# Performance work log

Measured on AMD Instinct MI355X. Metric: run time of the kernel, lower is better.

The kernel has to match this reference:

```python
import jax, jax.numpy as jnp
import numpy as np

D_MODEL = 1024
NUM_EXPERTS = 16
TOP_K = 2
TOP_C = 4  # min(E, max(4, 2*top_k))
TAU = 1.0
RANK = 64  # max(4, d_model // 16)


def _stable_softmax(v):
    m = jnp.max(v, axis=-1, keepdims=True)
    e = jnp.exp(v - m)
    return e / (jnp.sum(e, axis=-1, keepdims=True) + 1e-12)


def setup_inputs() -> dict:
    key = jax.random.key(0)
    ks = jax.random.split(key, 8)
    B, D, E, R = 16384, D_MODEL, NUM_EXPERTS, RANK
    x = jax.random.normal(ks[0], (B, D), dtype=jnp.float32)
    W_enc = jax.random.normal(ks[1], (D, D), dtype=jnp.float32) * (1.0 / np.sqrt(D))
    b_enc = jnp.zeros((D,), dtype=jnp.float32)
    W_gate = jax.random.normal(ks[2], (E, D), dtype=jnp.float32) * (1.0 / np.sqrt(D))
    U = jax.random.normal(ks[3], (E, R, D), dtype=jnp.float32) * (1.0 / np.sqrt(D))
    V = jax.random.normal(ks[4], (E, D, R), dtype=jnp.float32) * (1.0 / np.sqrt(R))
    gamma = jnp.ones((E,), dtype=jnp.float32)
    return {"x": x, "W_enc": W_enc, "b_enc": b_enc, "W_gate": W_gate,
            "U": U, "V": V, "gamma": gamma}


def reference(x, W_enc, b_enc, W_gate, U, V, gamma):
    # shared encoder
    encoded = x @ W_enc.T + b_enc                      # [B, D]
    # gating: logits -> top_c -> top_k -> softmax over selected logits
    logits = (encoded @ W_gate.T) / TAU                # [B, E]
    topc_vals, topc_idx = jax.lax.top_k(logits, TOP_C)
    topk_vals, pos_in_c = jax.lax.top_k(topc_vals, TOP_K)
    topk_idx = jnp.take_along_axis(topc_idx, pos_in_c, axis=1)  # [B, K]
    topk_w = _stable_softmax(topk_vals)                # [B, K], all > 1e-12
    # dense per-(token, expert) combine weight (equivalent to gather/scatter)
    B = x.shape[0]
    w_dense = jnp.zeros((B, NUM_EXPERTS), dtype=x.dtype)
    w_dense = w_dense.at[jnp.arange(B)[:, None], topk_idx].add(topk_w)
    # low-rank experts: delta_e(x) = gamma_e * silu(x U_e^T) V_e^T
    s = jax.nn.silu(jnp.einsum('bd,erd->ber', encoded, U))        # [B, E, R]
    coef = w_dense * gamma[None, :]                               # [B, E]
    delta = jnp.einsum('ber,edr->bd', s * coef[..., None], V)     # [B, D]
    # y = encoded + sum_k w_k * (expert(x) - x)  with expert(x)-x = delta_e
    return encoded + delta
```

## Files before the change

### kernel.cpp

```cpp
#include <hip/hip_runtime.h>
#include <hip/hip_bf16.h>

#define D_DIM 1024
#define NE 16
#define RK 64
#define NTOK 16384

typedef __bf16 bf16;
typedef __bf16 bf16x8 __attribute__((ext_vector_type(8)));
typedef __bf16 bf16x4 __attribute__((ext_vector_type(4)));
typedef float f32x4 __attribute__((ext_vector_type(4)));

__device__ __forceinline__ void gload16(const void* g, void* l) {
  __builtin_amdgcn_global_load_lds((const __attribute__((address_space(1))) unsigned int*)g,
                                   (__attribute__((address_space(3))) unsigned int*)l,
                                   16, 0, 0);
}

__global__ void k_cast(const float* __restrict__ s, bf16* __restrict__ d, int n4) {
  int i = blockIdx.x * blockDim.x + threadIdx.x;
  if (i >= n4) return;
  float4 v = ((const float4*)s)[i];
  bf16x4 o = { (bf16)v.x, (bf16)v.y, (bf16)v.z, (bf16)v.w };
  ((bf16x4*)d)[i] = o;
}

__global__ void k_castv(const float* __restrict__ V, bf16* __restrict__ Vb2) {
  int id = blockIdx.x * 256 + threadIdx.x;
  int d = id & 1023;
  int rb = (id >> 10) & 7;
  int e = id >> 13;
  const float* src = V + ((size_t)(e * 1024 + d)) * 64 + rb * 8;
  float4 v0 = *(const float4*)src;
  float4 v1 = *(const float4*)(src + 4);
  bf16x8 o = { (bf16)v0.x, (bf16)v0.y, (bf16)v0.z, (bf16)v0.w,
               (bf16)v1.x, (bf16)v1.y, (bf16)v1.z, (bf16)v1.w };
  *(bf16x8*)(Vb2 + (size_t)id * 8) = o;
}

__global__ void k_gmat(const float* __restrict__ Wg, const float* __restrict__ We,
                       float* __restrict__ Gt2) {
  int d = blockIdx.x * 256 + threadIdx.x;
  int e = blockIdx.y;
  int j0 = blockIdx.z * 128;
  double a0 = 0.0, a1 = 0.0, a2 = 0.0, a3 = 0.0;
  for (int j = j0; j < j0 + 128; j += 4) {
    a0 += (double)Wg[e * D_DIM + j + 0] * (double)We[(size_t)(j + 0) * D_DIM + d];
    a1 += (double)Wg[e * D_DIM + j + 1] * (double)We[(size_t)(j + 1) * D_DIM + d];
    a2 += (double)Wg[e * D_DIM + j + 2] * (double)We[(size_t)(j + 2) * D_DIM + d];
    a3 += (double)Wg[e * D_DIM + j + 3] * (double)We[(size_t)(j + 3) * D_DIM + d];
  }
  atomicAdd(&Gt2[(d >> 2) * 64 + e * 4 + (d & 3)], (float)((a0 + a1) + (a2 + a3)));
}

__global__ void k_bgate(const float* __restrict__ Wg, const float* __restrict__ be,
                        float* __restrict__ bg) {
  __shared__ double red[256];
  int e = blockIdx.x, t = threadIdx.x;
  double a = 0.0;
  for (int j = t; j < D_DIM; j += 256) a += (double)Wg[e * D_DIM + j] * (double)be[j];
  red[t] = a; __syncthreads();
  for (int s = 128; s > 0; s >>= 1) { if (t < s) red[t] += red[t + s]; __syncthreads(); }
  if (t == 0) bg[e] = (float)red[0];
}

__global__ __launch_bounds__(256) void k_gatecast(const float* __restrict__ x,
                                                  const float* __restrict__ Gt2,
                                                  const float* __restrict__ bg,
                                                  const float* __restrict__ gamma,
                                                  bf16* __restrict__ xb,
                                                  int* __restrict__ pk,
                                                  float2* __restrict__ wpair) {
  __shared__ float bufx[8][1024];
  __shared__ float Ls[4 * 2 * NE];
  int tid = threadIdx.x;
  int wv = tid >> 6, lane = tid & 63;
  int g = lane & 15;
  int s = lane >> 4;
  int tokbase = blockIdx.x * 8 + wv * 2;

  const float* xr0 = x + (size_t)tokbase * D_DIM;
#pragma unroll
  for (int c = 0; c < 4; ++c) {
    gload16(xr0 + c * 256 + lane * 4, &bufx[wv * 2][c * 256 + lane * 4]);
    gload16(xr0 + D_DIM + c * 256 + lane * 4, &bufx[wv * 2 + 1][c * 256 + lane * 4]);
  }

  const float* Gq = Gt2 + s * 64 + g * 4;
  const float* b0p = &bufx[wv * 2][s * 4];
  const float* b1p = &bufx[wv * 2 + 1][s * 4];
  float acc0 = 0.0f, acc1 = 0.0f;
  float4 gv = *(const float4*)Gq;
  for (int it = 0; it < 64; ++it) {
    int nx = (it < 63) ? it + 1 : 0;
    float4 gn = *(const float4*)(Gq + (size_t)nx * 256);
    float4 x0 = *(const float4*)(b0p + it * 16);
    float4 x1 = *(const float4*)(b1p + it * 16);
    acc0 += x0.x * gv.x + x0.y * gv.y + x0.z * gv.z + x0.w * gv.w;
    acc1 += x1.x * gv.x + x1.y * gv.y + x1.z * gv.z + x1.w * gv.w;
    gv = gn;
  }
  acc0 += __shfl_xor(acc0, 16); acc0 += __shfl_xor(acc0, 32);
  acc1 += __shfl_xor(acc1, 16); acc1 += __shfl_xor(acc1, 32);
  if (s == 0) {
    Ls[wv * 32 + g] = acc0;
    Ls[wv * 32 + 16 + g] = acc1;
  }

#pragma unroll
  for (int t = 0; t < 2; ++t) {
    const float4* src = (const float4*)&bufx[wv * 2 + t][0];
    bf16x4* dst = (bf16x4*)(xb + (size_t)(tokbase + t) * D_DIM);
#pragma unroll
    for (int r = 0; r < 4; ++r) {
      float4 v = src[lane + 64 * r];
      bf16x4 o = { (bf16)v.x, (bf16)v.y, (bf16)v.z, (bf16)v.w };
      dst[lane + 64 * r] = o;
    }
  }
  __syncthreads();

  if (lane < 2) {
    int t = lane;
    int tok = tokbase + t;
    const float* lrow = &Ls[wv * 32 + t * 16];
    float v1 = -1e30f, v2 = -1e30f; int i1 = 0, i2 = 0;
#pragma unroll
    for (int e = 0; e < NE; ++e) {
      float v = lrow[e] + bg[e];
      if (v > v1) { v2 = v1; i2 = i1; v1 = v; i1 = e; }
      else if (v > v2) { v2 = v; i2 = e; }
    }
    float e1 = expf(v2 - v1);
    float den = 1.0f + e1 + 1e-12f;
    float w0 = (1.0f / den) * gamma[i1];
    float w1 = (e1 / den) * gamma[i2];
    pk[tok] = i1 | (i2 << 8);
    wpair[tok] = make_float2(w0, w1);
  }
}

__global__ __launch_bounds__(256) void k_scatter(const int* __restrict__ pk,
                                                 const float2* __restrict__ wpair,
                                                 int* __restrict__ cnt,
                                                 int* __restrict__ lists,
                                                 float* __restrict__ wl) {
  __shared__ int lc[32];
  __shared__ int base[32];
  __shared__ int lc2[32];
  int tid = threadIdx.x;
  int tok = blockIdx.x * 256 + tid;
  if (tid < 32) { lc[tid] = 0; lc2[tid] = 0; }
  __syncthreads();
  int p = pk[tok];
  float2 w = wpair[tok];
  int b0 = p & 0xff;
  int b1 = 16 + ((p >> 8) & 0xff);
  atomicAdd(&lc[b0], 1);
  atomicAdd(&lc[b1], 1);
  __syncthreads();
  if (tid < 32 && lc[tid] > 0) base[tid] = atomicAdd(&cnt[tid], lc[tid]);
  __syncthreads();
  int r0 = base[b0] + atomicAdd(&lc2[b0], 1);
  lists[(size_t)b0 * NTOK + r0] = tok;
  wl[(size_t)b0 * NTOK + r0] = w.x;
  int r1 = base[b1] + atomicAdd(&lc2[b1], 1);
  lists[(size_t)b1 * NTOK + r1] = tok;
  wl[(size_t)b1 * NTOK + r1] = w.y;
}

__global__ void k_btab(const int* __restrict__ cnt, int2* __restrict__ btab,
                       int* __restrict__ nblk) {
  int lane = threadIdx.x;
  int nb = (lane < 32) ? ((cnt[lane] + 63) >> 6) : 0;
  int pfx = nb;
  for (int off = 1; off < 32; off <<= 1) {
    int v = __shfl_up(pfx, off);
    if (lane >= off) pfx += v;
  }
  int start = pfx - nb;
  if (lane < 32) {
    int c = cnt[lane];
    int i = 0;
    for (int t0 = 0; t0 < c; t0 += 64, ++i)
      btab[start + i] = make_int2(lane, t0);
  }
  if (lane == 31) *nblk = pfx;
}

__global__ __launch_bounds__(512, 1) void k_encgemm(const bf16* __restrict__ A,
                                                    const bf16* __restrict__ W,
                                                    const float* __restrict__ bias,
                                                    bf16* __restrict__ encb) {
  __shared__ bf16 As[256 * 64];
  __shared__ bf16 Bs[256 * 64];
  int tid = threadIdx.x;
  int w = blockIdx.x;
  int bm = (w & 63) * 256;
  int bn = (w >> 6) * 256;
  int lane = tid & 63, wv = tid >> 6;
  int wm = (wv >> 2) * 128, wn = (wv & 3) * 64;
  int srow = tid >> 3;
  int sc = tid & 7;
  int cs = sc ^ (srow & 7);
  int fr = lane & 15, fk = (lane >> 4) * 8;
  f32x4 acc[8][4] = {};
  for (int k0 = 0; k0 < D_DIM; k0 += 64) {
    __syncthreads();
#pragma unroll
    for (int p = 0; p < 4; ++p) {
      int r = p * 64 + srow;
      gload16(A + (size_t)(bm + r) * D_DIM + k0 + cs * 8, &As[r * 64 + sc * 8]);
    }
#pragma unroll
    for (int p = 0; p < 4; ++p) {
      int r = p * 64 + srow;
      gload16(W + (size_t)(bn + r) * D_DIM + k0 + cs * 8, &Bs[r * 64 + sc * 8]);
    }
    __syncthreads();
#pragma unroll
    for (int kk = 0; kk < 2; ++kk) {
      bf16x8 af[8], bv[4];
#pragma unroll
      for (int m = 0; m < 8; ++m) {
        int row = wm + m * 16 + fr;
        af[m] = *(const bf16x8*)&As[(row * 64 + kk * 32 + fk) ^ ((row & 7) << 3)];
      }
#pragma unroll
      for (int n = 0; n < 4; ++n) {
        int row = wn + n * 16 + fr;
        bv[n] = *(const bf16x8*)&Bs[(row * 64 + kk * 32 + fk) ^ ((row & 7) << 3)];
      }
#pragma unroll
      for (int m = 0; m < 8; ++m)
#pragma unroll
        for (int n = 0; n < 4; ++n)
          acc[m][n] = __builtin_amdgcn_mfma_f32_16x16x32_bf16(af[m], bv[n], acc[m][n], 0, 0, 0);
    }
  }
  int rg = (lane >> 4) * 4;
#pragma unroll
  for (int n = 0; n < 4; ++n) {
    int col = bn + wn + n * 16 + fr;
    float bval = bias[col];
#pragma unroll
    for (int m = 0; m < 8; ++m) {
#pragma unroll
      for (int r = 0; r < 4; ++r) {
        int row = bm + wm + m * 16 + rg + r;
        encb[(size_t)row * D_DIM + col] = (bf16)(acc[m][n][r] + bval);
      }
    }
  }
}

__global__ __launch_bounds__(256) void k_expert(const bf16* __restrict__ encb,
                                                const bf16* __restrict__ Ub,
                                                const bf16* __restrict__ Vb2,
                                                const int* __restrict__ cnt,
                                                const int* __restrict__ lists,
                                                const float* __restrict__ wl,
                                                const int2* __restrict__ btab,
                                                const int* __restrict__ nblk,
                                                bf16* __restrict__ d0,
                                                bf16* __restrict__ d1) {
  int bid = blockIdx.x;
  if (bid >= *nblk) return;
  int2 bt = btab[bid];
  int bin = bt.x, t0 = bt.y;
  int slot = bin >> 4, e = bin & 15;
  int c = cnt[bin];
  int nrows = c - t0; if (nrows > 64) nrows = 64;
  const int* tl = lists + (size_t)bin * NTOK + t0;
  const float* wlp = wl + (size_t)bin * NTOK + t0;

  __shared__ int toks[64];
  __shared__ float coefs[64];
  __shared__ bf16 As[64 * 64];
  __shared__ bf16 Us[64 * 64];
  __shared__ bf16 Ss[64 * 64];

  int tid = threadIdx.x;
  if (tid < 64) {
    int rr = tid < nrows ? tid : nrows - 1;
    toks[tid] = tl[rr];
    coefs[tid] = tid < nrows ? wlp[tid] : 0.0f;
  }
  __syncthreads();

  int lane = tid & 63, wv = tid >> 6;
  int srow = tid >> 3, scol = (tid & 7) * 8;
  int fr = lane & 15, fk = (lane >> 4) * 8;
  size_t tokA0 = (size_t)toks[srow] * D_DIM;
  size_t tokA1 = (size_t)toks[32 + srow] * D_DIM;
  const bf16* Ue = Ub + (size_t)e * RK * D_DIM;
  f32x4 acc1[4] = {};

  for (int k0 = 0; k0 < D_DIM; k0 += 64) {
    __syncthreads();
    gload16(encb + tokA0 + k0 + scol, &As[srow * 64 + scol]);
    gload16(encb + tokA1 + k0 + scol, &As[(32 + srow) * 64 + scol]);
    gload16(Ue + (size_t)srow * D_DIM + k0 + scol, &Us[srow * 64 + scol]);
    gload16(Ue + (size_t)(32 + srow) * D_DIM + k0 + scol, &Us[(32 + srow) * 64 + scol]);
    __syncthreads();
#pragma unroll
    for (int kk = 0; kk < 2; ++kk) {
      bf16x8 af = *(const bf16x8*)&As[(wv * 16 + fr) * 64 + kk * 32 + fk];
#pragma unroll
      for (int n = 0; n < 4; ++n) {
        bf16x8 bv = *(const bf16x8*)&Us[(n * 16 + fr) * 64 + kk * 32 + fk];
        acc1[n] = __builtin_amdgcn_mfma_f32_16x16x32_bf16(af, bv, acc1[n], 0, 0, 0);
      }
    }
  }
  int rg = (lane >> 4) * 4;
#pragma unroll
  for (int n = 0; n < 4; ++n)
#pragma unroll
    for (int r = 0; r < 4; ++r) {
      int row = wv * 16 + rg + r;
      float v = acc1[n][r];
      float s = v / (1.0f + __expf(-v));
      Ss[row * 64 + n * 16 + fr] = (bf16)(s * coefs[row]);
    }
  __syncthreads();
  bf16x8 a2[4][2];
#pragma unroll
  for (int m = 0; m < 4; ++m)
#pragma unroll
    for (int kk = 0; kk < 2; ++kk)
      a2[m][kk] = *(const bf16x8*)&Ss[(m * 16 + fr) * 64 + kk * 32 + fk];

  const bf16* Ve2 = Vb2 + (size_t)e * RK * D_DIM;
  bf16* dst = slot ? d1 : d0;
  int rb0 = lane >> 4;
  int colbase = wv * 256;
  for (int nj = 0; nj < 16; ++nj) {
    int dcol = colbase + nj * 16 + fr;
    bf16x8 b0 = *(const bf16x8*)&Ve2[((size_t)rb0 * D_DIM + dcol) * 8];
    bf16x8 b1 = *(const bf16x8*)&Ve2[((size_t)(rb0 + 4) * D_DIM + dcol) * 8];
#pragma unroll
    for (int m = 0; m < 4; ++m) {
      f32x4 a = {};
      a = __builtin_amdgcn_mfma_f32_16x16x32_bf16(a2[m][0], b0, a, 0, 0, 0);
      a = __builtin_amdgcn_mfma_f32_16x16x32_bf16(a2[m][1], b1, a, 0, 0, 0);
#pragma unroll
      for (int r = 0; r < 4; ++r) {
        int row = m * 16 + rg + r;
        if (row < nrows) {
          dst[(size_t)toks[row] * D_DIM + dcol] = (bf16)a[r];
        }
      }
    }
  }
}

__global__ __launch_bounds__(256) void k_final(float* __restrict__ out,
                                               const bf16* __restrict__ encb,
                                               const bf16* __restrict__ d0,
                                               const bf16* __restrict__ d1) {
  size_t i = ((size_t)blockIdx.x * 256 + threadIdx.x) * 8;
  bf16x8 e = *(const bf16x8*)(encb + i);
  bf16x8 a = *(const bf16x8*)(d0 + i);
  bf16x8 b = *(const bf16x8*)(d1 + i);
  float4 o0, o1;
  o0.x = (float)e[0] + (float)a[0] + (float)b[0];
  o0.y = (float)e[1] + (float)a[1] + (float)b[1];
  o0.z = (float)e[2] + (float)a[2] + (float)b[2];
  o0.w = (float)e[3] + (float)a[3] + (float)b[3];
  o1.x = (float)e[4] + (float)a[4] + (float)b[4];
  o1.y = (float)e[5] + (float)a[5] + (float)b[5];
  o1.z = (float)e[6] + (float)a[6] + (float)b[6];
  o1.w = (float)e[7] + (float)a[7] + (float)b[7];
  *(float4*)(out + i) = o0;
  *(float4*)(out + i + 4) = o1;
}

extern "C" void kernel_launch(void* const* d_in, const int* in_sizes, int n_in,
                              void* d_out, int out_size, void* d_ws, size_t ws_size,
                              hipStream_t stream) {
  const float* x   = (const float*)d_in[0];
  const float* We  = (const float*)d_in[1];
  const float* be  = (const float*)d_in[2];
  const float* Wg  = (const float*)d_in[3];
  const float* U   = (const float*)d_in[4];
  const float* V   = (const float*)d_in[5];
  const float* gam = (const float*)d_in[6];
  float* out = (float*)d_out;
  char* ws = (char*)d_ws;

  int*    cnt  = (int*)(ws + 0);
  float*  Gt2  = (float*)(ws + 256);
  float*  bg   = (float*)(ws + 66048);
  int2*   btab = (int2*)(ws + 66176);
  int*    nblk = (int*)(ws + 70656);
  bf16*   xb   = (bf16*)(ws + 131072);
  bf16*   d0   = (bf16*)(ws + 131072);
  bf16*   encb = (bf16*)(ws + 131072 + 33554432);
  char*   base = ws + 131072 + 2 * 33554432;
  bf16*   Wb   = (bf16*)(base);
  bf16*   Ubf  = (bf16*)(base + 2097152);
  bf16*   Vb2  = (bf16*)(base + 2 * 2097152);
  int*    lists= (int*)(base + 3 * 2097152);
  float*  wl   = (float*)(base + 4 * 2097152);
  int*    pk   = (int*)(base + 5 * 2097152);
  float2* wpr  = (float2*)(base + 5 * 2097152 + 131072);
  bf16*   d1   = (bf16*)(base + 5 * 2097152 + 131072 + 131072 + 131072);

  hipMemsetAsync(ws, 0, 66048, stream);

  k_cast<<<1024, 256, 0, stream>>>(We, Wb, 1048576 / 4);
  k_cast<<<1024, 256, 0, stream>>>(U, Ubf, 1048576 / 4);
  k_castv<<<512, 256, 0, stream>>>(V, Vb2);

  dim3 gg(4, 16, 8);
  k_gmat<<<gg, 256, 0, stream>>>(Wg, We, Gt2);
  k_bgate<<<16, 256, 0, stream>>>(Wg, be, bg);

  k_gatecast<<<2048, 256, 0, stream>>>(x, Gt2, bg, gam, xb, pk, wpr);
  k_scatter<<<64, 256, 0, stream>>>(pk, wpr, cnt, lists, wl);
  k_btab<<<1, 64, 0, stream>>>(cnt, btab, nblk);

  k_encgemm<<<256, 512, 0, stream>>>(xb, Wb, be, encb);

  k_expert<<<544, 256, 0, stream>>>(encb, Ubf, Vb2, cnt, lists, wl, btab, nblk, d0, d1);
  k_final<<<8192, 256, 0, stream>>>(out, encb, d0, d1);
}
```

Before: 183.8 us.

## Double-buffer encoder and expert GEMMs, stage epilogue stores through LDS

The encoder GEMM now uses a 32-wide K step with two LDS buffers, so global-to-LDS loads for the next tile are issued before the MFMAs on the current tile, and the XOR swizzle is dropped. The expert kernel gets a double-buffered, swizzled first GEMM. Both epilogues stage bf16 results in padded per-wave LDS tiles so global writes become vectorized row-contiguous stores instead of scattered 2-byte stores. The aim is to hide load latency and cut store transactions, at the cost of more LDS per block and possible bank conflicts from the unswizzled 32-wide encoder tiles.

```diff
diff --git a/kernel.cpp b/kernel.cpp
--- a/kernel.cpp
+++ b/kernel.cpp
@@ -192,64 +192,78 @@
                                                     const bf16* __restrict__ W,
                                                     const float* __restrict__ bias,
                                                     bf16* __restrict__ encb) {
-  __shared__ bf16 As[256 * 64];
-  __shared__ bf16 Bs[256 * 64];
+  __shared__ char smem[65536];
+  bf16* const AsB = (bf16*)smem;
+  bf16* const BsB = (bf16*)(smem + 32768);
   int tid = threadIdx.x;
   int w = blockIdx.x;
   int bm = (w & 63) * 256;
   int bn = (w >> 6) * 256;
   int lane = tid & 63, wv = tid >> 6;
   int wm = (wv >> 2) * 128, wn = (wv & 3) * 64;
-  int srow = tid >> 3;
-  int sc = tid & 7;
-  int cs = sc ^ (srow & 7);
+  int srow = tid >> 2;
+  int sc = (tid & 3) * 8;
   int fr = lane & 15, fk = (lane >> 4) * 8;
   f32x4 acc[8][4] = {};
-  for (int k0 = 0; k0 < D_DIM; k0 += 64) {
+
+  {
+    bf16* as = AsB; bf16* bs = BsB;
+    gload16(A + (size_t)(bm + srow) * D_DIM + sc, &as[srow * 32 + sc]);
+    gload16(A + (size_t)(bm + 128 + srow) * D_DIM + sc, &as[(128 + srow) * 32 + sc]);
+    gload16(W + (size_t)(bn + srow) * D_DIM + sc, &bs[srow * 32 + sc]);
+    gload16(W + (size_t)(bn + 128 + srow) * D_DIM + sc, &bs[(128 + srow) * 32 + sc]);
+  }
+  __syncthreads();
+
+  for (int k0 = 0; k0 < D_DIM; k0 += 32) {
+    int cur = (k0 >> 5) & 1;
+    if (k0 + 32 < D_DIM) {
+      int kn = k0 + 32;
+      bf16* as = AsB + (cur ^ 1) * 8192;
+      bf16* bs = BsB + (cur ^ 1) * 8192;
+      gload16(A + (size_t)(bm + srow) * D_DIM + kn + sc, &as[srow * 32 + sc]);
+      gload16(A + (size_t)(bm + 128 + srow) * D_DIM + kn + sc, &as[(128 + srow) * 32 + sc]);
+      gload16(W + (size_t)(bn + srow) * D_DIM + kn + sc, &bs[srow * 32 + sc]);
+      gload16(W + (size_t)(bn + 128 + srow) * D_DIM + kn + sc, &bs[(128 + srow) * 32 + sc]);
+    }
+    const bf16* as = AsB + cur * 8192;
+    const bf16* bs = BsB + cur * 8192;
+    bf16x8 af[8], bv[4];
+#pragma unroll
+    for (int m = 0; m < 8; ++m)
+      af[m] = *(const bf16x8*)&as[(wm + m * 16 + fr) * 32 + fk];
+#pragma unroll
+    for (int n = 0; n < 4; ++n)
+      bv[n] = *(const bf16x8*)&bs[(wn + n * 16 + fr) * 32 + fk];
+#pragma unroll
+    for (int m = 0; m < 8; ++m)
+#pragma unroll
+      for (int n = 0; n < 4; ++n)
+        acc[m][n] = __builtin_amdgcn_mfma_f32_16x16x32_bf16(af[m], bv[n], acc[m][n], 0, 0, 0);
     __syncthreads();
-#pragma unroll
-    for (int p = 0; p < 4; ++p) {
-      int r = p * 64 + srow;
-      gload16(A + (size_t)(bm + r) * D_DIM + k0 + cs * 8, &As[r * 64 + sc * 8]);
-    }
-#pragma unroll
-    for (int p = 0; p < 4; ++p) {
-      int r = p * 64 + srow;
-      gload16(W + (size_t)(bn + r) * D_DIM + k0 + cs * 8, &Bs[r * 64 + sc * 8]);
-    }
-    __syncthreads();
-#pragma unroll
-    for (int kk = 0; kk < 2; ++kk) {
-      bf16x8 af[8], bv[4];
-#pragma unroll
-      for (int m = 0; m < 8; ++m) {
-        int row = wm + m * 16 + fr;
-        af[m] = *(const bf16x8*)&As[(row * 64 + kk * 32 + fk) ^ ((row & 7) << 3)];
+  }
+
+  int rg = (lane >> 4) * 4;
+  bf16* tb = (bf16*)smem + wv * 2176;
+#pragma unroll
+  for (int h = 0; h < 4; ++h) {
+#pragma unroll
+    for (int mi = 0; mi < 2; ++mi) {
+      int m = h * 2 + mi;
+#pragma unroll
+      for (int n = 0; n < 4; ++n) {
+        float bval = bias[bn + wn + n * 16 + fr];
+#pragma unroll
+        for (int r = 0; r < 4; ++r)
+          tb[(mi * 16 + rg + r) * 68 + n * 16 + fr] = (bf16)(acc[m][n][r] + bval);
       }
-#pragma unroll
-      for (int n = 0; n < 4; ++n) {
-        int row = wn + n * 16 + fr;
-        bv[n] = *(const bf16x8*)&Bs[(row * 64 + kk * 32 + fk) ^ ((row & 7) << 3)];
-      }
-#pragma unroll
-      for (int m = 0; m < 8; ++m)
-#pragma unroll
-        for (int n = 0; n < 4; ++n)
-          acc[m][n] = __builtin_amdgcn_mfma_f32_16x16x32_bf16(af[m], bv[n], acc[m][n], 0, 0, 0);
-    }
-  }
-  int rg = (lane >> 4) * 4;
-#pragma unroll
-  for (int n = 0; n < 4; ++n) {
-    int col = bn + wn + n * 16 + fr;
-    float bval = bias[col];
-#pragma unroll
-    for (int m = 0; m < 8; ++m) {
-#pragma unroll
-      for (int r = 0; r < 4; ++r) {
-        int row = bm + wm + m * 16 + rg + r;
-        encb[(size_t)row * D_DIM + col] = (bf16)(acc[m][n][r] + bval);
-      }
+    }
+#pragma unroll
+    for (int it2 = 0; it2 < 8; ++it2) {
+      int row = it2 * 4 + (lane >> 4);
+      int c4 = (lane & 15) * 4;
+      *(ushort4*)&encb[(size_t)(bm + wm + h * 32 + row) * D_DIM + bn + wn + c4] =
+        *(const ushort4*)&tb[row * 68 + c4];
     }
   }
 }
@@ -276,9 +290,10 @@
 
   __shared__ int toks[64];
   __shared__ float coefs[64];
-  __shared__ bf16 As[64 * 64];
-  __shared__ bf16 Us[64 * 64];
+  __shared__ bf16 As[2][64 * 64];
+  __shared__ bf16 Us[2][64 * 64];
   __shared__ bf16 Ss[64 * 64];
+  __shared__ bf16 xtrb[4][64 * 34];
 
   int tid = threadIdx.x;
   if (tid < 64) {
@@ -289,30 +304,45 @@
   __syncthreads();
 
   int lane = tid & 63, wv = tid >> 6;
-  int srow = tid >> 3, scol = (tid & 7) * 8;
+  int srow = tid >> 3;
+  int sc8 = tid & 7;
+  int cs = (sc8 ^ (srow & 7)) * 8;
+  int scol = sc8 * 8;
   int fr = lane & 15, fk = (lane >> 4) * 8;
   size_t tokA0 = (size_t)toks[srow] * D_DIM;
   size_t tokA1 = (size_t)toks[32 + srow] * D_DIM;
   const bf16* Ue = Ub + (size_t)e * RK * D_DIM;
   f32x4 acc1[4] = {};
 
+  gload16(encb + tokA0 + cs, &As[0][srow * 64 + scol]);
+  gload16(encb + tokA1 + cs, &As[0][(32 + srow) * 64 + scol]);
+  gload16(Ue + (size_t)srow * D_DIM + cs, &Us[0][srow * 64 + scol]);
+  gload16(Ue + (size_t)(32 + srow) * D_DIM + cs, &Us[0][(32 + srow) * 64 + scol]);
+  __syncthreads();
+
   for (int k0 = 0; k0 < D_DIM; k0 += 64) {
-    __syncthreads();
-    gload16(encb + tokA0 + k0 + scol, &As[srow * 64 + scol]);
-    gload16(encb + tokA1 + k0 + scol, &As[(32 + srow) * 64 + scol]);
-    gload16(Ue + (size_t)srow * D_DIM + k0 + scol, &Us[srow * 64 + scol]);
-    gload16(Ue + (size_t)(32 + srow) * D_DIM + k0 + scol, &Us[(32 + srow) * 64 + scol]);
-    __syncthreads();
+    int cur = (k0 >> 6) & 1;
+    if (k0 + 64 < D_DIM) {
+      int kn = k0 + 64;
+      gload16(encb + tokA0 + kn + cs, &As[cur ^ 1][srow * 64 + scol]);
+      gload16(encb + tokA1 + kn + cs, &As[cur ^ 1][(32 + srow) * 64 + scol]);
+      gload16(Ue + (size_t)srow * D_DIM + kn + cs, &Us[cur ^ 1][srow * 64 + scol]);
+      gload16(Ue + (size_t)(32 + srow) * D_DIM + kn + cs, &Us[cur ^ 1][(32 + srow) * 64 + scol]);
+    }
+    int arow = wv * 16 + fr;
+    int sw = (fr & 7) << 3;
 #pragma unroll
     for (int kk = 0; kk < 2; ++kk) {
-      bf16x8 af = *(const bf16x8*)&As[(wv * 16 + fr) * 64 + kk * 32 + fk];
+      bf16x8 af = *(const bf16x8*)&As[cur][(arow * 64 + kk * 32 + fk) ^ sw];
 #pragma unroll
       for (int n = 0; n < 4; ++n) {
-        bf16x8 bv = *(const bf16x8*)&Us[(n * 16 + fr) * 64 + kk * 32 + fk];
+        bf16x8 bv = *(const bf16x8*)&Us[cur][((n * 16 + fr) * 64 + kk * 32 + fk) ^ sw];
         acc1[n] = __builtin_amdgcn_mfma_f32_16x16x32_bf16(af, bv, acc1[n], 0, 0, 0);
       }
     }
-  }
+    __syncthreads();
+  }
+
   int rg = (lane >> 4) * 4;
 #pragma unroll
   for (int n = 0; n < 4; ++n)
@@ -335,22 +365,31 @@
   bf16* dst = slot ? d1 : d0;
   int rb0 = lane >> 4;
   int colbase = wv * 256;
-  for (int nj = 0; nj < 16; ++nj) {
-    int dcol = colbase + nj * 16 + fr;
-    bf16x8 b0 = *(const bf16x8*)&Ve2[((size_t)rb0 * D_DIM + dcol) * 8];
-    bf16x8 b1 = *(const bf16x8*)&Ve2[((size_t)(rb0 + 4) * D_DIM + dcol) * 8];
-#pragma unroll
-    for (int m = 0; m < 4; ++m) {
-      f32x4 a = {};
-      a = __builtin_amdgcn_mfma_f32_16x16x32_bf16(a2[m][0], b0, a, 0, 0, 0);
-      a = __builtin_amdgcn_mfma_f32_16x16x32_bf16(a2[m][1], b1, a, 0, 0, 0);
-#pragma unroll
-      for (int r = 0; r < 4; ++r) {
-        int row = m * 16 + rg + r;
-        if (row < nrows) {
-          dst[(size_t)toks[row] * D_DIM + dcol] = (bf16)a[r];
-        }
+  bf16* tb = xtrb[wv];
+  for (int njb = 0; njb < 8; ++njb) {
+#pragma unroll
+    for (int nj2 = 0; nj2 < 2; ++nj2) {
+      int nj = njb * 2 + nj2;
+      int dcol = colbase + nj * 16 + fr;
+      bf16x8 b0 = *(const bf16x8*)&Ve2[((size_t)rb0 * D_DIM + dcol) * 8];
+      bf16x8 b1 = *(const bf16x8*)&Ve2[((size_t)(rb0 + 4) * D_DIM + dcol) * 8];
+#pragma unroll
+      for (int m = 0; m < 4; ++m) {
+        f32x4 a = {};
+        a = __builtin_amdgcn_mfma_f32_16x16x32_bf16(a2[m][0], b0, a, 0, 0, 0);
+        a = __builtin_amdgcn_mfma_f32_16x16x32_bf16(a2[m][1], b1, a, 0, 0, 0);
+#pragma unroll
+        for (int r = 0; r < 4; ++r)
+          tb[(m * 16 + rg + r) * 34 + nj2 * 16 + fr] = (bf16)a[r];
       }
+    }
+#pragma unroll
+    for (int it2 = 0; it2 < 16; ++it2) {
+      int row = it2 * 4 + (lane >> 4);
+      int c2 = (lane & 15) * 2;
+      if (row < nrows)
+        *(ushort2*)&dst[(size_t)toks[row] * D_DIM + colbase + njb * 32 + c2] =
+          *(const ushort2*)&tb[row * 34 + c2];
     }
   }
 }
```

Measured after the change: 193.7 us. 1.05x slower.
